# Kernel optimization log

Hardware: AMD Instinct MI355X
Metric: run time of the kernel (lower is better)

The kernel has to match this reference:

```python
import jax, jax.numpy as jnp
import numpy as np

H = 8            # num_heads
WIN = 128        # num_windows (sliding-window half-width)
B, T, C = 2, 4096, 512


def setup_inputs() -> dict:
    key = jax.random.key(0)
    k1, k2, k3 = jax.random.split(key, 3)
    x = jax.random.normal(k1, (B, T, C), dtype=jnp.float32)
    W_qkv = jax.random.normal(k2, (C, 3 * C), dtype=jnp.float32) * (C ** -0.5)
    W_out = jax.random.normal(k3, (C, C), dtype=jnp.float32) * (C ** -0.5)
    b_out = jnp.zeros((C,), dtype=jnp.float32)
    return {"x": x, "W_qkv": W_qkv, "W_out": W_out, "b_out": b_out}


def reference(x, W_qkv, W_out, b_out):
    Bx, Tx, Cx = x.shape
    hd = Cx // H
    scale = hd ** -0.5
    # qkv projection -> [B, T, 3, H, hd]
    qkv = (x @ W_qkv).reshape(Bx, Tx, 3, H, hd)
    q, k, v = qkv[:, :, 0], qkv[:, :, 1], qkv[:, :, 2]  # each [B, T, H, hd]
    # attention scores [B, H, T, T]
    scores = jnp.einsum('bihd,bjhd->bhij', q, k) * scale
    idx = jnp.arange(Tx)
    band = jnp.abs(idx[:, None] - idx[None, :]) <= WIN  # [T, T] bool
    scores = jnp.where(band[None, None], scores, jnp.float32(-jnp.inf))
    attn = jax.nn.softmax(scores, axis=-1)
    # dropout is identity in eval mode (p handled by config; omitted)
    out = jnp.einsum('bhij,bjhd->bihd', attn, v).reshape(Bx, Tx, Cx)
    return out @ W_out + b_out
```

## Files before the change

kernel.cpp:

```cpp
#include <hip/hip_runtime.h>
#include <stdint.h>

typedef unsigned short ushort_t;
typedef __attribute__((ext_vector_type(8))) __bf16 bf16x8;
typedef __attribute__((ext_vector_type(8))) unsigned short ushortx8;
typedef __attribute__((ext_vector_type(4))) float floatx4;
typedef __attribute__((ext_vector_type(4))) unsigned int uint4v;

__device__ inline ushort_t f2bf(float f) {
  union { float f; unsigned u; } v; v.f = f;
  unsigned r = v.u + 0x7FFFu + ((v.u >> 16) & 1u);
  return (ushort_t)(r >> 16);
}

__device__ inline floatx4 mfma16(bf16x8 a, bf16x8 b, floatx4 c) {
  return __builtin_amdgcn_mfma_f32_16x16x32_bf16(a, b, c, 0, 0, 0);
}

__device__ inline void gload_lds16(const ushort_t* g, ushort_t* l) {
  __builtin_amdgcn_global_load_lds((__attribute__((address_space(1))) void*)(void*)(g),
                                   (__attribute__((address_space(3))) void*)(l),
                                   16, 0, 0);
}

__global__ __launch_bounds__(256)
void k_prep(const float* __restrict__ x, ushort_t* __restrict__ xb,
            const float* __restrict__ Wqkv, ushort_t* __restrict__ wqkvT,
            const float* __restrict__ Wout, ushort_t* __restrict__ woutT) {
  int bx = blockIdx.x, tid = threadIdx.x;
  if (bx < 4096) {
    int i = (bx * 256 + tid) * 4;
    float4 v = *(const float4*)(x + i);
    ushort4 o;
    o.x = f2bf(v.x); o.y = f2bf(v.y); o.z = f2bf(v.z); o.w = f2bf(v.w);
    *(ushort4*)(xb + i) = o;
    return;
  }
  __shared__ float tile[32][33];
  const float* src; ushort_t* dst; int N, id;
  if (bx < 4096 + 768) { id = bx - 4096; src = Wqkv; dst = wqkvT; N = 1536; }
  else                 { id = bx - 4864; src = Wout; dst = woutT; N = 512;  }
  int k0 = (id & 15) * 32, n0 = (id >> 4) * 32;
  int c = tid & 31, r0 = tid >> 5;
#pragma unroll
  for (int i = 0; i < 4; ++i) {
    int r = r0 + i * 8;
    tile[r][c] = src[(size_t)(k0 + r) * N + n0 + c];
  }
  __syncthreads();
#pragma unroll
  for (int i = 0; i < 4; ++i) {
    int r = r0 + i * 8;
    dst[(size_t)(n0 + r) * 512 + k0 + c] = f2bf(tile[c][r]);
  }
}

__global__ __launch_bounds__(256)
void k_gemm1(const ushort_t* __restrict__ A, const ushort_t* __restrict__ Bt,
             ushort_t* __restrict__ qd, ushort_t* __restrict__ kd,
             ushort_t* __restrict__ vtd) {
  __shared__ __align__(16) ushort_t smem[12288];
  ushort_t* As = smem;
  ushort_t* Bs = smem + 4096;
  const int tid = threadIdx.x;
  const int w = tid >> 6, l = tid & 63;
  const int lr = l & 15, lq = l >> 4;
  const int m0 = blockIdx.x * 64, n0 = blockIdx.y * 128;
  const int wm = w >> 1, wn = w & 1;

  floatx4 acc[2][4];
#pragma unroll
  for (int i = 0; i < 2; ++i)
#pragma unroll
    for (int j = 0; j < 4; ++j) acc[i][j] = (floatx4)0.0f;

  for (int k0 = 0; k0 < 512; k0 += 64) {
#pragma unroll
    for (int i = 0; i < 6; ++i) {
      int idx = w * 6 + i;
      if (idx < 8) {
        int blk = idx >> 1, half = idx & 1;
        gload_lds16(A + (size_t)(m0 + blk * 16 + lr) * 512 + k0 + half * 32 + lq * 8,
                    &As[blk * 1024 + half * 512]);
      } else {
        int j = idx - 8, blk = j >> 1, half = j & 1;
        gload_lds16(Bt + (size_t)(n0 + blk * 16 + lr) * 512 + k0 + half * 32 + lq * 8,
                    &Bs[blk * 1024 + half * 512]);
      }
    }
    __syncthreads();
#pragma unroll
    for (int half = 0; half < 2; ++half) {
      bf16x8 af[2], bfr[4];
#pragma unroll
      for (int i = 0; i < 2; ++i)
        af[i] = *(const bf16x8*)&As[(wm * 2 + i) * 1024 + half * 512 + l * 8];
#pragma unroll
      for (int j = 0; j < 4; ++j)
        bfr[j] = *(const bf16x8*)&Bs[(wn * 4 + j) * 1024 + half * 512 + l * 8];
#pragma unroll
      for (int i = 0; i < 2; ++i)
#pragma unroll
        for (int j = 0; j < 4; ++j) acc[i][j] = mfma16(af[i], bfr[j], acc[i][j]);
    }
    __syncthreads();
  }

  if (blockIdx.y < 8) {
#pragma unroll
    for (int i = 0; i < 2; ++i)
#pragma unroll
      for (int j = 0; j < 4; ++j) {
        int col = wn * 64 + j * 16 + lr;
#pragma unroll
        for (int r = 0; r < 4; ++r) {
          int row = wm * 32 + i * 16 + lq * 4 + r;
          smem[row * 136 + col] = f2bf(acc[i][j][r]);
        }
      }
    __syncthreads();
#pragma unroll
    for (int p = 0; p < 4; ++p) {
      int row = p * 16 + (tid >> 4), c8 = (tid & 15) * 8;
      ushortx8 vv = *(const ushortx8*)&smem[row * 136 + c8];
      int n = n0 + c8;
      ushort_t* dst = (n >> 9) ? kd : qd;
      int h = (n >> 6) & 7, d = n & 63;
      int m = m0 + row, b = m >> 12, t = m & 4095;
      *(ushortx8*)&dst[(((size_t)(b * 8 + h)) * 4096 + t) * 64 + d] = vv;
    }
  } else {
#pragma unroll
    for (int i = 0; i < 2; ++i)
#pragma unroll
      for (int j = 0; j < 4; ++j) {
        int dcol = wn * 64 + j * 16 + lr;
        int trow = wm * 32 + i * 16 + lq * 4;
        ushort4 pv;
        pv.x = f2bf(acc[i][j][0]); pv.y = f2bf(acc[i][j][1]);
        pv.z = f2bf(acc[i][j][2]); pv.w = f2bf(acc[i][j][3]);
        *(ushort4*)&smem[dcol * 72 + trow] = pv;
      }
    __syncthreads();
#pragma unroll
    for (int p = 0; p < 4; ++p) {
      int row = p * 32 + (tid >> 3), c8 = (tid & 7) * 8;
      ushortx8 vv = *(const ushortx8*)&smem[row * 72 + c8];
      int n = n0 + row, h = (n >> 6) & 7, d = n & 63;
      int m = m0 + c8, b = m >> 12, t = m & 4095;
      *(ushortx8*)&vtd[(((size_t)(b * 8 + h)) * 64 + d) * 4096 + t] = vv;
    }
  }
}

__global__ __launch_bounds__(256)
void k_gemm2(const ushort_t* __restrict__ A, const ushort_t* __restrict__ Bt,
             float* __restrict__ outf, const float* __restrict__ bias) {
  __shared__ __align__(16) char smemc[33792];
  ushort_t* As = (ushort_t*)smemc;
  ushort_t* Bs = (ushort_t*)(smemc + 8192);
  float* Cs = (float*)smemc;
  const int tid = threadIdx.x;
  const int w = tid >> 6, l = tid & 63;
  const int lr = l & 15, lq = l >> 4;
  const int m0 = blockIdx.x * 64, n0 = blockIdx.y * 128;
  const int wm = w >> 1, wn = w & 1;

  floatx4 acc[2][4];
#pragma unroll
  for (int i = 0; i < 2; ++i)
#pragma unroll
    for (int j = 0; j < 4; ++j) acc[i][j] = (floatx4)0.0f;

  for (int k0 = 0; k0 < 512; k0 += 64) {
#pragma unroll
    for (int i = 0; i < 6; ++i) {
      int idx = w * 6 + i;
      if (idx < 8) {
        int blk = idx >> 1, half = idx & 1;
        gload_lds16(A + (size_t)(m0 + blk * 16 + lr) * 512 + k0 + half * 32 + lq * 8,
                    &As[blk * 1024 + half * 512]);
      } else {
        int j = idx - 8, blk = j >> 1, half = j & 1;
        gload_lds16(Bt + (size_t)(n0 + blk * 16 + lr) * 512 + k0 + half * 32 + lq * 8,
                    &Bs[blk * 1024 + half * 512]);
      }
    }
    __syncthreads();
#pragma unroll
    for (int half = 0; half < 2; ++half) {
      bf16x8 af[2], bfr[4];
#pragma unroll
      for (int i = 0; i < 2; ++i)
        af[i] = *(const bf16x8*)&As[(wm * 2 + i) * 1024 + half * 512 + l * 8];
#pragma unroll
      for (int j = 0; j < 4; ++j)
        bfr[j] = *(const bf16x8*)&Bs[(wn * 4 + j) * 1024 + half * 512 + l * 8];
#pragma unroll
      for (int i = 0; i < 2; ++i)
#pragma unroll
        for (int j = 0; j < 4; ++j) acc[i][j] = mfma16(af[i], bfr[j], acc[i][j]);
    }
    __syncthreads();
  }

#pragma unroll
  for (int i = 0; i < 2; ++i)
#pragma unroll
    for (int j = 0; j < 4; ++j) {
      int col = wn * 64 + j * 16 + lr;
      float bv = bias[n0 + col];
#pragma unroll
      for (int r = 0; r < 4; ++r) {
        int row = wm * 32 + i * 16 + lq * 4 + r;
        Cs[row * 132 + col] = acc[i][j][r] + bv;
      }
    }
  __syncthreads();
#pragma unroll
  for (int p = 0; p < 4; ++p) {
    int row = p * 16 + (tid >> 4), c = (tid & 15) * 8;
    float4 v0 = *(const float4*)&Cs[row * 132 + c];
    float4 v1 = *(const float4*)&Cs[row * 132 + c + 4];
    float* op = &outf[(size_t)(m0 + row) * 512 + n0 + c];
    *(float4*)op = v0;
    *(float4*)(op + 4) = v1;
  }
}

__global__ __launch_bounds__(256)
void k_attn(const ushort_t* __restrict__ qa, const ushort_t* __restrict__ ka,
            const ushort_t* __restrict__ vta, ushort_t* __restrict__ ao) {
  __shared__ __align__(16) ushort_t S[20 * 1024];
  const int tid = threadIdx.x, w = tid >> 6, l = tid & 63;
  const int lr = l & 15, lq = l >> 4;
  const int g = blockIdx.x;
  const int xcd = g & 7, j = g >> 3;
  const int bh = xcd * 2 + (j & 1);
  const int qt0 = (j >> 1) * 64;
  const int qrow = qt0 + w * 16;

  const ushort_t* kbase = ka + (size_t)bh * 4096 * 64;
#pragma unroll
  for (int i = 0; i < 10; ++i) {
    int idx = w * 10 + i, blk = idx >> 1, half = idx & 1;
    int row = qt0 - 128 + blk * 16 + lr;
    row = min(max(row, 0), 4095);
    gload_lds16(kbase + (size_t)row * 64 + half * 32 + lq * 8, &S[blk * 1024 + half * 512]);
  }

  const ushort_t* qp = qa + ((size_t)bh * 4096 + qrow + lr) * 64 + lq * 8;
  bf16x8 qf0 = *(const bf16x8*)qp;
  bf16x8 qf1 = *(const bf16x8*)(qp + 32);

  __syncthreads();

  const float Cc = 0.125f * 1.4426950408889634f;
  uint2 pk[18];
  pk[17].x = 0u; pk[17].y = 0u;
  float ps = 0.f;
#pragma unroll
  for (int kt = 0; kt < 17; ++kt) {
    const ushort_t* kp = &S[(w + kt) * 1024 + l * 8];
    bf16x8 kf0 = *(const bf16x8*)kp;
    bf16x8 kf1 = *(const bf16x8*)(kp + 512);
    floatx4 s = (floatx4)0.0f;
    s = mfma16(kf0, qf0, s);
    s = mfma16(kf1, qf1, s);
    float p[4];
#pragma unroll
    for (int r = 0; r < 4; ++r) {
      int r_rel = kt * 16 + lq * 4 + r;
      int kj = qrow - 128 + r_rel;
      bool ok = (kj >= 0) && (kj < 4096) && (r_rel >= lr) && (r_rel - lr <= 256);
      float e = ok ? exp2f(s[r] * Cc) : 0.f;
      ps += e;
      p[r] = e;
    }
    pk[kt].x = (unsigned)f2bf(p[0]) | ((unsigned)f2bf(p[1]) << 16);
    pk[kt].y = (unsigned)f2bf(p[2]) | ((unsigned)f2bf(p[3]) << 16);
  }

  ps += __shfl_xor(ps, 16, 64);
  ps += __shfl_xor(ps, 32, 64);
  float inv = __builtin_amdgcn_rcpf(ps);
  float invr[4];
#pragma unroll
  for (int r = 0; r < 4; ++r) invr[r] = __shfl(inv, lq * 4 + r, 64);

  __syncthreads();

  const ushort_t* vbase = vta + (size_t)bh * 64 * 4096;
#pragma unroll
  for (int i = 0; i < 10; ++i) {
    int t = w * 10 + i, kt2 = t >> 2, nt = t & 3;
    int d = nt * 16 + lr;
    int key = qt0 - 128 + kt2 * 32 + lq * 8;
    key = min(max(key, 0), 4088);
    gload_lds16(vbase + (size_t)d * 4096 + key, &S[t * 512]);
  }

  const int srcA = ((l >> 4) & 1) * 32 + lr;
  const int srcB = srcA + 16;
  const bool selhi = (l & 32) != 0;
  bf16x8 pu9[9];
#pragma unroll
  for (int kk = 0; kk < 9; ++kk) {
    unsigned e0 = __shfl(pk[2 * kk].x, srcA, 64);
    unsigned e1 = __shfl(pk[2 * kk].y, srcA, 64);
    unsigned e2 = __shfl(pk[2 * kk].x, srcB, 64);
    unsigned e3 = __shfl(pk[2 * kk].y, srcB, 64);
    unsigned o0 = __shfl(pk[2 * kk + 1].x, srcA, 64);
    unsigned o1 = __shfl(pk[2 * kk + 1].y, srcA, 64);
    unsigned o2 = __shfl(pk[2 * kk + 1].x, srcB, 64);
    unsigned o3 = __shfl(pk[2 * kk + 1].y, srcB, 64);
    union { uint4v u; bf16x8 b; } pu;
    pu.u[0] = selhi ? o0 : e0;
    pu.u[1] = selhi ? o1 : e1;
    pu.u[2] = selhi ? o2 : e2;
    pu.u[3] = selhi ? o3 : e3;
    pu9[kk] = pu.b;
  }

  __syncthreads();

  floatx4 oacc[4];
#pragma unroll
  for (int nt = 0; nt < 4; ++nt) oacc[nt] = (floatx4)0.0f;
#pragma unroll
  for (int kk = 0; kk < 9; ++kk) {
    int keyrel = w * 16 + kk * 32 + lq * 8;
    keyrel = min(keyrel, 312);
    int kt2 = keyrel >> 5, seg = (keyrel >> 3) & 3;
    const ushort_t* vsp = &S[kt2 * 2048 + seg * 128 + lr * 8];
#pragma unroll
    for (int nt = 0; nt < 4; ++nt) {
      bf16x8 vf = *(const bf16x8*)(vsp + nt * 512);
      oacc[nt] = mfma16(pu9[kk], vf, oacc[nt]);
    }
  }

  __syncthreads();

#pragma unroll
  for (int nt = 0; nt < 4; ++nt)
#pragma unroll
    for (int r = 0; r < 4; ++r)
      S[(w * 16 + lq * 4 + r) * 72 + nt * 16 + lr] = f2bf(oacc[nt][r] * invr[r]);
  __syncthreads();

  int b = bh >> 3, h = bh & 7;
#pragma unroll
  for (int p = 0; p < 2; ++p) {
    int row = p * 32 + (tid >> 3), c8 = (tid & 7) * 8;
    ushortx8 vv = *(const ushortx8*)&S[row * 72 + c8];
    *(ushortx8*)&ao[((size_t)(b * 4096 + qt0 + row)) * 512 + h * 64 + c8] = vv;
  }
}

extern "C" void kernel_launch(void* const* d_in, const int* in_sizes, int n_in,
                              void* d_out, int out_size, void* d_ws, size_t ws_size,
                              hipStream_t stream) {
  const float* x    = (const float*)d_in[0];
  const float* Wqkv = (const float*)d_in[1];
  const float* Wout = (const float*)d_in[2];
  const float* bout = (const float*)d_in[3];
  float* out = (float*)d_out;
  char* ws = (char*)d_ws;
  const size_t MB = 1024 * 1024;

  ushort_t* xb    = (ushort_t*)(ws);
  ushort_t* wqkvT = (ushort_t*)(ws + 8 * MB);
  ushort_t* woutT = (ushort_t*)(ws + 9 * MB + MB/2);
  ushort_t* q     = (ushort_t*)(ws + 10 * MB);
  ushort_t* k     = (ushort_t*)(ws + 18 * MB);
  ushort_t* vt    = (ushort_t*)(ws + 26 * MB);
  ushort_t* ao    = xb;

  k_prep<<<5120, 256, 0, stream>>>(x, xb, Wqkv, wqkvT, Wout, woutT);
  k_gemm1<<<dim3(128, 12), 256, 0, stream>>>(xb, wqkvT, q, k, vt);
  k_attn<<<1024, 256, 0, stream>>>(q, k, vt, ao);
  k_gemm2<<<dim3(128, 4), 256, 0, stream>>>(ao, woutT, out, bout);
}
```

Before: 146.5 us.

## Double-buffer LDS staging in QKV and output projection GEMMs

Both projection GEMMs now prefetch the next two K-tiles into alternating LDS buffers with direct global-to-LDS loads. Raw vmcnt waits and s_barrier replace the full __syncthreads, so memory latency can overlap with MFMA work. This doubles LDS per block, which may lower occupancy, and correctness depends on the hand-placed waitcnt counts.

```diff
diff --git a/kernel.cpp b/kernel.cpp
--- a/kernel.cpp
+++ b/kernel.cpp
@@ -6,6 +6,9 @@
 typedef __attribute__((ext_vector_type(8))) unsigned short ushortx8;
 typedef __attribute__((ext_vector_type(4))) float floatx4;
 typedef __attribute__((ext_vector_type(4))) unsigned int uint4v;
+
+#define WAITCNT_VM(N) asm volatile("s_waitcnt vmcnt(" #N ")" ::: "memory")
+#define BARRIER_RAW() asm volatile("s_barrier" ::: "memory")
 
 __device__ inline ushort_t f2bf(float f) {
   union { float f; unsigned u; } v; v.f = f;
@@ -55,13 +58,29 @@
   }
 }
 
+__device__ inline void stage_ab(const ushort_t* __restrict__ A, const ushort_t* __restrict__ Bt,
+                                ushort_t* buf, int m0, int n0, int k0,
+                                int w, int lr, int lq) {
+#pragma unroll
+  for (int i = 0; i < 6; ++i) {
+    int idx = w * 6 + i;
+    if (idx < 8) {
+      int blk = idx >> 1, half = idx & 1;
+      gload_lds16(A + (size_t)(m0 + blk * 16 + lr) * 512 + k0 + half * 32 + lq * 8,
+                  &buf[blk * 1024 + half * 512]);
+    } else {
+      int j = idx - 8, blk = j >> 1, half = j & 1;
+      gload_lds16(Bt + (size_t)(n0 + blk * 16 + lr) * 512 + k0 + half * 32 + lq * 8,
+                  &buf[4096 + blk * 1024 + half * 512]);
+    }
+  }
+}
+
 __global__ __launch_bounds__(256)
 void k_gemm1(const ushort_t* __restrict__ A, const ushort_t* __restrict__ Bt,
              ushort_t* __restrict__ qd, ushort_t* __restrict__ kd,
              ushort_t* __restrict__ vtd) {
-  __shared__ __align__(16) ushort_t smem[12288];
-  ushort_t* As = smem;
-  ushort_t* Bs = smem + 4096;
+  __shared__ __align__(16) ushort_t smem[24576];
   const int tid = threadIdx.x;
   const int w = tid >> 6, l = tid & 63;
   const int lr = l & 15, lq = l >> 4;
@@ -74,21 +93,15 @@
 #pragma unroll
     for (int j = 0; j < 4; ++j) acc[i][j] = (floatx4)0.0f;
 
-  for (int k0 = 0; k0 < 512; k0 += 64) {
-#pragma unroll
-    for (int i = 0; i < 6; ++i) {
-      int idx = w * 6 + i;
-      if (idx < 8) {
-        int blk = idx >> 1, half = idx & 1;
-        gload_lds16(A + (size_t)(m0 + blk * 16 + lr) * 512 + k0 + half * 32 + lq * 8,
-                    &As[blk * 1024 + half * 512]);
-      } else {
-        int j = idx - 8, blk = j >> 1, half = j & 1;
-        gload_lds16(Bt + (size_t)(n0 + blk * 16 + lr) * 512 + k0 + half * 32 + lq * 8,
-                    &Bs[blk * 1024 + half * 512]);
-      }
-    }
-    __syncthreads();
+  stage_ab(A, Bt, smem,         m0, n0, 0,  w, lr, lq);
+  stage_ab(A, Bt, smem + 12288, m0, n0, 64, w, lr, lq);
+
+#pragma unroll
+  for (int it = 0; it < 8; ++it) {
+    if (it < 7) { WAITCNT_VM(6); } else { WAITCNT_VM(0); }
+    BARRIER_RAW();
+    const ushort_t* As = smem + (it & 1) * 12288;
+    const ushort_t* Bs = As + 4096;
 #pragma unroll
     for (int half = 0; half < 2; ++half) {
       bf16x8 af[2], bfr[4];
@@ -103,8 +116,11 @@
 #pragma unroll
         for (int j = 0; j < 4; ++j) acc[i][j] = mfma16(af[i], bfr[j], acc[i][j]);
     }
-    __syncthreads();
-  }
+    BARRIER_RAW();
+    if (it < 6)
+      stage_ab(A, Bt, smem + (it & 1) * 12288, m0, n0, (it + 2) * 64, w, lr, lq);
+  }
+  __syncthreads();
 
   if (blockIdx.y < 8) {
 #pragma unroll
@@ -156,9 +172,8 @@
 __global__ __launch_bounds__(256)
 void k_gemm2(const ushort_t* __restrict__ A, const ushort_t* __restrict__ Bt,
              float* __restrict__ outf, const float* __restrict__ bias) {
-  __shared__ __align__(16) char smemc[33792];
-  ushort_t* As = (ushort_t*)smemc;
-  ushort_t* Bs = (ushort_t*)(smemc + 8192);
+  __shared__ __align__(16) char smemc[49152];
+  ushort_t* sm = (ushort_t*)smemc;
   float* Cs = (float*)smemc;
   const int tid = threadIdx.x;
   const int w = tid >> 6, l = tid & 63;
@@ -172,21 +187,15 @@
 #pragma unroll
     for (int j = 0; j < 4; ++j) acc[i][j] = (floatx4)0.0f;
 
-  for (int k0 = 0; k0 < 512; k0 += 64) {
-#pragma unroll
-    for (int i = 0; i < 6; ++i) {
-      int idx = w * 6 + i;
-      if (idx < 8) {
-        int blk = idx >> 1, half = idx & 1;
-        gload_lds16(A + (size_t)(m0 + blk * 16 + lr) * 512 + k0 + half * 32 + lq * 8,
-                    &As[blk * 1024 + half * 512]);
-      } else {
-        int j = idx - 8, blk = j >> 1, half = j & 1;
-        gload_lds16(Bt + (size_t)(n0 + blk * 16 + lr) * 512 + k0 + half * 32 + lq * 8,
-                    &Bs[blk * 1024 + half * 512]);
-      }
-    }
-    __syncthreads();
+  stage_ab(A, Bt, sm,         m0, n0, 0,  w, lr, lq);
+  stage_ab(A, Bt, sm + 12288, m0, n0, 64, w, lr, lq);
+
+#pragma unroll
+  for (int it = 0; it < 8; ++it) {
+    if (it < 7) { WAITCNT_VM(6); } else { WAITCNT_VM(0); }
+    BARRIER_RAW();
+    const ushort_t* As = sm + (it & 1) * 12288;
+    const ushort_t* Bs = As + 4096;
 #pragma unroll
     for (int half = 0; half < 2; ++half) {
       bf16x8 af[2], bfr[4];
@@ -201,8 +210,11 @@
 #pragma unroll
         for (int j = 0; j < 4; ++j) acc[i][j] = mfma16(af[i], bfr[j], acc[i][j]);
     }
-    __syncthreads();
-  }
+    BARRIER_RAW();
+    if (it < 6)
+      stage_ab(A, Bt, sm + (it & 1) * 12288, m0, n0, (it + 2) * 64, w, lr, lq);
+  }
+  __syncthreads();
 
 #pragma unroll
   for (int i = 0; i < 2; ++i)
```

New measurement: 144.5 us. No clear change (-1.4%).
